# Performance work log

Measured on AMD Instinct MI355X. Metric: run time of the kernel, lower is better.

Reference implementation:

```python
import jax, jax.numpy as jnp
import numpy as np

SUB_NO, T_NO, T_DATA, E_NO, I_NO = 20, 201, 100000, 800, 200


def _build_c_den():
    # binary-tree dendrite topology: children of node p are 2p+1, 2p+2 (indices > parent,
    # so the reverse-order recursion in forward() is valid)
    C = np.zeros((SUB_NO, SUB_NO), np.float32)
    for p in range(SUB_NO):
        for c in (2 * p + 1, 2 * p + 2):
            if c < SUB_NO:
                C[p, c] = 1.0
    return jnp.asarray(C)


def setup_inputs() -> dict:
    key = jax.random.key(0)
    ks = jax.random.split(key, 8)
    S_e = jax.random.uniform(ks[0], (T_DATA, E_NO), dtype=jnp.float32)
    S_i = jax.random.uniform(ks[1], (T_DATA, I_NO), dtype=jnp.float32)
    # one-hot synapse -> subunit assignment matrices (fixed, greedy=False)
    ae = jax.random.randint(ks[2], (E_NO,), 0, SUB_NO)
    ai = jax.random.randint(ks[3], (I_NO,), 0, SUB_NO)
    C_syn_e = jax.nn.one_hot(ae, SUB_NO, dtype=jnp.float32).T  # (sub_no, E_no)
    C_syn_i = jax.nn.one_hot(ai, SUB_NO, dtype=jnp.float32).T  # (sub_no, I_no)
    W_syn = jax.random.uniform(ks[4], (SUB_NO, 2, 2), dtype=jnp.float32) * 0.05
    W_syn = W_syn.at[:, :, 1].multiply(-1.0)  # inhibitory weights negative
    Tau_syn = jnp.tile(jnp.array([1.1, 3.1], jnp.float32).reshape(1, 2, 1), (SUB_NO, 1, 2))
    Delta_syn = jax.random.uniform(ks[5], (SUB_NO, 2, 2), dtype=jnp.float32)
    W_sub = jax.random.uniform(ks[6], (SUB_NO,), dtype=jnp.float32)
    Theta = jnp.zeros((SUB_NO,), jnp.float32)
    V_o = jax.random.normal(ks[7], (1,), dtype=jnp.float32)
    return {"S_e": S_e, "S_i": S_i, "C_syn_e": C_syn_e, "C_syn_i": C_syn_i,
            "C_den": _build_c_den(), "W_syn": W_syn, "Tau_syn": Tau_syn,
            "Delta_syn": Delta_syn, "W_sub": W_sub, "Theta": Theta, "V_o": V_o}


def _alpha_kernels(W_syn, Tau_syn, Delta_syn):
    # sum of 2 alpha functions per subunit, separately for e (c=0) and i (c=1)
    t = jnp.arange(T_NO, dtype=jnp.float32)
    td = jnp.maximum(t[None, None, None, :] - Delta_syn[..., None], 0.0)  # (sub,2,2,T_no)
    tt = td / jnp.exp(Tau_syn)[..., None]
    part = tt * jnp.exp(-tt) * W_syn[..., None]
    kern = part.sum(axis=1)  # sum over the 2 alpha components -> (sub,2,T_no)
    return kern[:, 0, :], kern[:, 1, :]  # e_kern, i_kern each (sub, T_no)


def _causal_grouped_conv(syn, kern):
    # syn: (T, sub), kern: (sub, T_no). Matches torch: flip kernel, left-pad T_no-1 zeros,
    # grouped valid cross-correlation -> causal conv, output (T, sub).
    sub, T_no = kern.shape
    x = jnp.pad(syn.T, ((0, 0), (T_no - 1, 0)))[None]      # (1, sub, T+T_no-1)
    k = jnp.flip(kern, 1)[:, None, :]                       # (sub, 1, T_no)
    y = jax.lax.conv_general_dilated(x, k, (1,), 'VALID',
                                     dimension_numbers=('NCH', 'OIH', 'NCH'),
                                     feature_group_count=sub)
    return y[0].T


def reference(S_e, S_i, C_syn_e, C_syn_i, C_den, W_syn, Tau_syn, Delta_syn, W_sub, Theta, V_o):
    syn_e = S_e @ C_syn_e.T  # (T, sub) aggregated excitatory input
    syn_i = S_i @ C_syn_i.T
    e_kern, i_kern = _alpha_kernels(W_syn, Tau_syn, Delta_syn)
    syn_in = _causal_grouped_conv(syn_e, e_kern) + _causal_grouped_conv(syn_i, i_kern)
    # dendritic tree recursion, leaves (high idx) to root (idx 0).
    # leaf gather/sum expressed as a masked matvec with the binary C_den row
    # (exactly equal to the original gather since C_den is 0/1).
    W_exp = jnp.exp(W_sub)
    sub_no = C_den.shape[0]
    sub_out = jnp.zeros_like(syn_in)  # (T, sub)
    for s in range(sub_no - 1, -1, -1):
        leaf_sum = sub_out @ (C_den[s] * W_exp)  # (T,)
        sub_out = sub_out.at[:, s].set(jnp.tanh(syn_in[:, s] + leaf_sum + Theta[s]))
    final_voltage = sub_out[:, 0] * W_exp[0] + V_o  # (T,) via broadcast of V_o[1]
    out_filters = jnp.vstack((e_kern, i_kern))  # double flip in torch cancels
    return final_voltage, out_filters, C_syn_e, C_syn_i
```

## Files before the change

kernel.cpp:

```cpp
#include <hip/hip_runtime.h>
#include <hip/hip_bf16.h>
#include <stdint.h>

constexpr int T    = 100000;
constexpr int TNO  = 201;
constexpr int KP   = 204;
constexpr int NSUB = 20;
constexpr int ENO  = 800;
constexpr int INO  = 200;
constexpr int NCS  = 40;

constexpr int OUT_FILT = T;
constexpr int OUT_CSE  = OUT_FILT + NCS * TNO;

constexpr int WS_KFLIP = 0;
constexpr int WS_OFFE  = 32640;
constexpr int WS_OFFI  = 32768;
constexpr int WS_PERME = 32896;
constexpr int WS_PERMI = 36096;
constexpr int WS_SYN   = 36928;
constexpr size_t WS_NEEDED_SPLIT = (size_t)WS_SYN + (size_t)NCS * T * 4;

__device__ __forceinline__ float u16f(unsigned short u) {
  return __uint_as_float((unsigned int)u << 16);
}
__device__ __forceinline__ float ldany(const void* p, int i, int f32) {
  return f32 ? ((const float*)p)[i] : u16f(((const unsigned short*)p)[i]);
}
__device__ __forceinline__ void stany(void* p, int i, float v, int f32) {
  if (f32) ((float*)p)[i] = v;
  else     ((__hip_bfloat16*)p)[i] = __float2bfloat16(v);
}
__device__ __forceinline__ float safe_tanh(float x) {
  return 1.f - 2.f / (expf(2.f * x) + 1.f);
}

__device__ __forceinline__ int detect_f32(const void* Se) {
  const uint32_t w = ((const uint32_t*)Se)[threadIdx.x & 63];
  return (__ballot((w & 0x8000u) != 0u) != 0ull) ? 1 : 0;
}

__global__ __launch_bounds__(256) void kern_setup(
    const void* __restrict__ Se,
    const void* __restrict__ Wsyn,
    const void* __restrict__ Tau,
    const void* __restrict__ Delta,
    const void* __restrict__ Cse,
    const void* __restrict__ Csi,
    void* __restrict__ out,
    float* __restrict__ kflip,
    int* __restrict__ offE, int* __restrict__ offI,
    int* __restrict__ permE, int* __restrict__ permI)
{
  __shared__ int cnt[NSUB], offsh[NSUB + 1], pos[ENO], asg[ENO];

  const int f32 = detect_f32(Se);
  const int tid = threadIdx.x;
  const int cs  = blockIdx.x;
  const int s   = cs % NSUB;
  const int c   = cs / NSUB;

  if (tid <= 200) {
    const float tau = (float)tid;
    float v = 0.f;
#pragma unroll
    for (int j = 0; j < 2; ++j) {
      const float W  = ldany(Wsyn , (s * 2 + j) * 2 + c, f32);
      const float Tu = ldany(Tau  , (s * 2 + j) * 2 + c, f32);
      const float De = ldany(Delta, (s * 2 + j) * 2 + c, f32);
      const float td = fmaxf(tau - De, 0.f);
      const float tt = td / expf(Tu);
      v += tt * expf(-tt) * W;
    }
    stany(out, OUT_FILT + cs * TNO + tid, v, f32);
    kflip[cs * KP + (200 - tid)] = v;
  } else if (tid < KP) {
    kflip[cs * KP + tid] = 0.f;
  }

  for (int idx = blockIdx.x * 256 + tid; idx < NSUB * (ENO + INO); idx += 40 * 256) {
    const float v = (idx < NSUB * ENO) ? ldany(Cse, idx, f32)
                                       : ldany(Csi, idx - NSUB * ENO, f32);
    stany(out, OUT_CSE + idx, v, f32);
  }

  if (blockIdx.x == 0) {
    if (tid < NSUB) cnt[tid] = 0;
    __syncthreads();
    for (int e = tid; e < ENO; e += 256) {
      int a = 0;
      for (int ss = 0; ss < NSUB; ++ss)
        if (ldany(Cse, ss * ENO + e, f32) > 0.5f) a = ss;
      asg[e] = a;
      pos[e] = atomicAdd(&cnt[a], 1);
    }
    __syncthreads();
    if (tid == 0) {
      int acc = 0;
      for (int ss = 0; ss < NSUB; ++ss) { offsh[ss] = acc; acc += cnt[ss]; }
      offsh[NSUB] = acc;
    }
    __syncthreads();
    if (tid <= NSUB) offE[tid] = offsh[tid];
    for (int e = tid; e < ENO; e += 256) permE[offsh[asg[e]] + pos[e]] = e;
    __syncthreads();
    if (tid < NSUB) cnt[tid] = 0;
    __syncthreads();
    for (int e = tid; e < INO; e += 256) {
      int a = 0;
      for (int ss = 0; ss < NSUB; ++ss)
        if (ldany(Csi, ss * INO + e, f32) > 0.5f) a = ss;
      asg[e] = a;
      pos[e] = atomicAdd(&cnt[a], 1);
    }
    __syncthreads();
    if (tid == 0) {
      int acc = 0;
      for (int ss = 0; ss < NSUB; ++ss) { offsh[ss] = acc; acc += cnt[ss]; }
      offsh[NSUB] = acc;
    }
    __syncthreads();
    if (tid <= NSUB) offI[tid] = offsh[tid];
    for (int e = tid; e < INO; e += 256) permI[offsh[asg[e]] + pos[e]] = e;
  }
}

constexpr int AR   = 8;
constexpr int FSTR = 1004;
constexpr int BSTR = 504;

__global__ __launch_bounds__(256) void kern_agg(
    const void* __restrict__ Se,
    const void* __restrict__ Si,
    const int* __restrict__ offE, const int* __restrict__ offI,
    const int* __restrict__ permE, const int* __restrict__ permI,
    float* __restrict__ syn)
{
  __shared__ alignas(16) uint32_t lds[AR * FSTR];
  __shared__ int sOffE[NSUB + 1], sOffI[NSUB + 1];
  __shared__ int sPermE[ENO], sPermI[INO];

  const int f32 = detect_f32(Se);
  const int tid = threadIdx.x;
  const int t0  = blockIdx.x * AR;

  for (int i = tid; i < ENO; i += 256) sPermE[i] = permE[i];
  for (int i = tid; i < INO; i += 256) sPermI[i] = permI[i];
  if (tid <= NSUB) { sOffE[tid] = offE[tid]; sOffI[tid] = offI[tid]; }

  if (f32) {
    const float4* gE4 = (const float4*)Se + (size_t)t0 * 200;
    const float4* gI4 = (const float4*)Si + (size_t)t0 * 50;
#pragma unroll
    for (int u = 0; u < 7; ++u) {
      const int idx = tid + u * 256;
      float4 v; int w;
      if (idx < 1600) { v = gE4[idx]; const int r = idx / 200;
                        w = r * FSTR + (idx - r * 200) * 4; }
      else            { const int j = idx - 1600; v = gI4[j]; const int r = j / 50;
                        w = r * FSTR + 800 + (j - r * 50) * 4; }
      *(float4*)&lds[w] = v;
    }
    {
      const int idx = tid + 1792;
      if (idx < 2000) {
        const int j = idx - 1600;
        const int r = j / 50;
        *(float4*)&lds[r * FSTR + 800 + (j - r * 50) * 4] = gI4[j];
      }
    }
  } else {
    const uint32_t* gE = (const uint32_t*)Se + (size_t)t0 * 400;
    const uint32_t* gI = (const uint32_t*)Si + (size_t)t0 * 100;
    for (int idx = tid; idx < AR * 500; idx += 256) {
      const int r = idx / 500;
      const int w = idx - r * 500;
      lds[r * BSTR + w] = (w < 400) ? gE[r * 400 + w] : gI[r * 100 + (w - 400)];
    }
  }
  __syncthreads();

  for (int task = tid; task < NCS * AR; task += 256) {
    const int cs = task >> 3, r = task & 7;
    float v = 0.f;
    if (f32) {
      const float* row = (const float*)lds + r * FSTR;
      if (cs < NSUB) {
        const int b0 = sOffE[cs], b1 = sOffE[cs + 1];
#pragma unroll 4
        for (int k = b0; k < b1; ++k) v += row[sPermE[k]];
      } else {
        const int ss = cs - NSUB;
        const int b0 = sOffI[ss], b1 = sOffI[ss + 1];
#pragma unroll 4
        for (int k = b0; k < b1; ++k) v += row[800 + sPermI[k]];
      }
    } else {
      const unsigned short* row = (const unsigned short*)lds + r * (BSTR * 2);
      if (cs < NSUB) {
        const int b0 = sOffE[cs], b1 = sOffE[cs + 1];
        for (int k = b0; k < b1; ++k) v += u16f(row[sPermE[k]]);
      } else {
        const int ss = cs - NSUB;
        const int b0 = sOffI[ss], b1 = sOffI[ss + 1];
        for (int k = b0; k < b1; ++k) v += u16f(row[800 + sPermI[k]]);
      }
    }
    syn[(size_t)cs * T + t0 + r] = v;
  }
}

template<int TTC, int SBSC>
__device__ __forceinline__ void conv_tree_core(
    float* sybuf, const float* __restrict__ kflip,
    const float* __restrict__ wexpS, const float* __restrict__ thetaS,
    const void* __restrict__ Vo,
    void* __restrict__ out, int t0, int tid, int f32)
{
  constexpr int GRP   = TTC / 4;
  constexpr int NTASK = NCS * GRP;
  constexpr int NPASS = NTASK / 640;
  static_assert(NTASK % 640 == 0, "task count must tile 640 threads");

  float acc[NPASS][4];
#pragma unroll
  for (int pass = 0; pass < NPASS; ++pass) {
    const int task = tid + pass * 640;
    const int cs   = task / GRP;
    const int r0   = (task % GRP) << 2;
    const float*  xb = &sybuf[cs * SBSC + r0];
    const float4* kf = (const float4*)(kflip + cs * KP);
    float4 cur = *(const float4*)xb;
    float a0 = 0.f, a1 = 0.f, a2 = 0.f, a3 = 0.f;
    for (int jb = 0; jb < KP; jb += 4) {
      const float4 nxt = *(const float4*)(xb + jb + 4);
      const float4 k   = kf[jb >> 2];
      a0 = fmaf(k.x, cur.x, a0); a1 = fmaf(k.x, cur.y, a1);
      a2 = fmaf(k.x, cur.z, a2); a3 = fmaf(k.x, cur.w, a3);
      a0 = fmaf(k.y, cur.y, a0); a1 = fmaf(k.y, cur.z, a1);
      a2 = fmaf(k.y, cur.w, a2); a3 = fmaf(k.y, nxt.x, a3);
      a0 = fmaf(k.z, cur.z, a0); a1 = fmaf(k.z, cur.w, a1);
      a2 = fmaf(k.z, nxt.x, a2); a3 = fmaf(k.z, nxt.y, a3);
      a0 = fmaf(k.w, cur.w, a0); a1 = fmaf(k.w, nxt.x, a1);
      a2 = fmaf(k.w, nxt.y, a2); a3 = fmaf(k.w, nxt.z, a3);
      cur = nxt;
    }
    acc[pass][0] = a0; acc[pass][1] = a1; acc[pass][2] = a2; acc[pass][3] = a3;
  }
  __syncthreads();
#pragma unroll
  for (int pass = 0; pass < NPASS; ++pass) {
    const int task = tid + pass * 640;
    const int cs   = task / GRP;
    const int r0   = (task % GRP) << 2;
    sybuf[cs * SBSC + r0 + 0] = acc[pass][0];
    sybuf[cs * SBSC + r0 + 1] = acc[pass][1];
    sybuf[cs * SBSC + r0 + 2] = acc[pass][2];
    sybuf[cs * SBSC + r0 + 3] = acc[pass][3];
  }
  __syncthreads();

  if (tid < TTC) {
    const int t = t0 + tid;
    if (t < T) {
      float so[NSUB];
#pragma unroll
      for (int ss = NSUB - 1; ss >= 0; --ss) {
        float x = sybuf[ss * SBSC + tid] + sybuf[(NSUB + ss) * SBSC + tid]
                + thetaS[ss];
        if (2 * ss + 1 < NSUB) x += wexpS[2 * ss + 1] * so[2 * ss + 1];
        if (2 * ss + 2 < NSUB) x += wexpS[2 * ss + 2] * so[2 * ss + 2];
        so[ss] = safe_tanh(x);
      }
      stany(out, t, so[0] * wexpS[0] + ldany(Vo, 0, f32), f32);
    }
  }
}

constexpr int TT2 = 128;
constexpr int SB2 = 336;

__global__ __launch_bounds__(640) void kern_conv_tree(
    const void* __restrict__ Se,
    const float* __restrict__ kflip,
    const float* __restrict__ syn,
    const void* __restrict__ Wsub,
    const void* __restrict__ ThetaP,
    const void* __restrict__ Vo,
    void* __restrict__ out)
{
  __shared__ alignas(16) float sybuf[NCS * SB2];
  __shared__ float wexpS[NSUB], thetaS[NSUB];
  const int f32 = detect_f32(Se);
  const int tid = threadIdx.x;
  const int t0  = blockIdx.x * TT2;

  if (tid < NSUB) {
    wexpS[tid]  = expf(ldany(Wsub, tid, f32));
    thetaS[tid] = ldany(ThetaP, tid, f32);
  }
  for (int idx = tid; idx < NCS * (TT2 + KP); idx += 640) {
    const int cs = idx / (TT2 + KP);
    const int i  = idx - cs * (TT2 + KP);
    const int g  = t0 - 200 + i;
    float v = 0.f;
    if (g >= 0 && g < T) v = syn[(size_t)cs * T + g];
    sybuf[cs * SB2 + i] = v;
  }
  __syncthreads();
  conv_tree_core<TT2, SB2>(sybuf, kflip, wexpS, thetaS, Vo, out, t0, tid, f32);
}

constexpr int TT1 = 64;
constexpr int SB1 = 272;

__global__ __launch_bounds__(640) void kern_fused(
    const void* __restrict__ Se,
    const void* __restrict__ Si,
    const float* __restrict__ kflip,
    const int* __restrict__ offE, const int* __restrict__ offI,
    const int* __restrict__ permE, const int* __restrict__ permI,
    const void* __restrict__ Wsub,
    const void* __restrict__ ThetaP,
    const void* __restrict__ Vo,
    void* __restrict__ out)
{
  __shared__ alignas(16) float    sybuf[NCS * SB1];
  __shared__ alignas(16) uint32_t stage[4008];
  __shared__ float wexpS[NSUB], thetaS[NSUB];
  __shared__ int sOffE[NSUB + 1], sOffI[NSUB + 1];
  __shared__ int sPermE[ENO], sPermI[INO];

  const int f32 = detect_f32(Se);
  const int tid = threadIdx.x;
  const int t0  = blockIdx.x * TT1;

  for (int i = tid; i < ENO; i += 640) sPermE[i] = permE[i];
  for (int i = tid; i < INO; i += 640) sPermI[i] = permI[i];
  if (tid <= NSUB) { sOffE[tid] = offE[tid]; sOffI[tid] = offI[tid]; }
  if (tid < NSUB) {
    wexpS[tid]  = expf(ldany(Wsub, tid, f32));
    thetaS[tid] = ldany(ThetaP, tid, f32);
  }

  if (!f32) {
    const uint32_t* SeU = (const uint32_t*)Se;
    const uint32_t* SiU = (const uint32_t*)Si;
    for (int c = 0; c < 34; ++c) {
      const int g0 = t0 - 200 + c * 8;
      for (int idx = tid; idx < 8 * 500; idx += 640) {
        const int r = idx / 500;
        const int w = idx - r * 500;
        const int g = g0 + r;
        uint32_t v = 0u;
        if (g >= 0 && g < T)
          v = (w < 400) ? SeU[(size_t)g * 400 + w] : SiU[(size_t)g * 100 + (w - 400)];
        stage[r * 501 + w] = v;
      }
      __syncthreads();
      if (tid < 320) {
        const int isI = tid >= 160;
        const int t2  = isI ? tid - 160 : tid;
        const int ss  = t2 >> 3, r = t2 & 7;
        const int i   = c * 8 + r;
        const unsigned short* row = (const unsigned short*)(stage + r * 501);
        float v = 0.f;
        if (!isI) {
          for (int k = sOffE[ss]; k < sOffE[ss + 1]; ++k) v += u16f(row[sPermE[k]]);
          sybuf[ss * SB1 + i] = v;
        } else {
          row += 800;
          for (int k = sOffI[ss]; k < sOffI[ss + 1]; ++k) v += u16f(row[sPermI[k]]);
          sybuf[(NSUB + ss) * SB1 + i] = v;
        }
      }
      __syncthreads();
    }
  } else {
    const uint32_t* SeU = (const uint32_t*)Se;
    const uint32_t* SiU = (const uint32_t*)Si;
    for (int c = 0; c < 68; ++c) {
      const int g0 = t0 - 200 + c * 4;
      for (int idx = tid; idx < 4 * 1000; idx += 640) {
        const int r = idx / 1000;
        const int w = idx - r * 1000;
        const int g = g0 + r;
        uint32_t v = 0u;
        if (g >= 0 && g < T)
          v = (w < 800) ? SeU[(size_t)g * 800 + w] : SiU[(size_t)g * 200 + (w - 800)];
        stage[r * 1001 + w] = v;
      }
      __syncthreads();
      if (tid < 160) {
        const int isI = tid >= 80;
        const int t2  = isI ? tid - 80 : tid;
        const int ss  = t2 >> 2, r = t2 & 3;
        const int i   = c * 4 + r;
        const float* row = (const float*)(stage + r * 1001);
        float v = 0.f;
        if (!isI) {
          for (int k = sOffE[ss]; k < sOffE[ss + 1]; ++k) v += row[sPermE[k]];
          sybuf[ss * SB1 + i] = v;
        } else {
          row += 800;
          for (int k = sOffI[ss]; k < sOffI[ss + 1]; ++k) v += row[sPermI[k]];
          sybuf[(NSUB + ss) * SB1 + i] = v;
        }
      }
      __syncthreads();
    }
  }
  conv_tree_core<TT1, SB1>(sybuf, kflip, wexpS, thetaS, Vo, out, t0, tid, f32);
}

extern "C" void kernel_launch(void* const* d_in, const int* in_sizes, int n_in,
                              void* d_out, int out_size, void* d_ws, size_t ws_size,
                              hipStream_t stream)
{
  const void* Se    = d_in[0];
  const void* Si    = d_in[1];
  const void* Cse   = d_in[2];
  const void* Csi   = d_in[3];
  const void* Wsyn  = d_in[5];
  const void* Tau   = d_in[6];
  const void* Delta = d_in[7];
  const void* Wsub  = d_in[8];
  const void* Theta = d_in[9];
  const void* Vo    = d_in[10];

  char* ws = (char*)d_ws;
  float* kflip = (float*)(ws + WS_KFLIP);
  int*   offE  = (int*)(ws + WS_OFFE);
  int*   offI  = (int*)(ws + WS_OFFI);
  int*   permE = (int*)(ws + WS_PERME);
  int*   permI = (int*)(ws + WS_PERMI);
  float* syn   = (float*)(ws + WS_SYN);

  kern_setup<<<dim3(NCS), dim3(256), 0, stream>>>(
      Se, Wsyn, Tau, Delta, Cse, Csi, d_out, kflip, offE, offI, permE, permI);

  if (ws_size >= WS_NEEDED_SPLIT) {
    kern_agg<<<dim3(T / AR), dim3(256), 0, stream>>>(
        Se, Si, offE, offI, permE, permI, syn);
    kern_conv_tree<<<dim3((T + TT2 - 1) / TT2), dim3(640), 0, stream>>>(
        Se, kflip, syn, Wsub, Theta, Vo, d_out);
  } else {
    kern_fused<<<dim3((T + TT1 - 1) / TT1), dim3(640), 0, stream>>>(
        Se, Si, kflip, offE, offI, permE, permI, Wsub, Theta, Vo, d_out);
  }
}
```

Measured before the change: 629.5 us.

## Make aggregation kernel persistent with register prefetch and in-block permutation build

The aggregation kernel becomes a persistent grid of 1024 blocks that loop over time tiles. In the f32 path each block prefetches the next tile into registers while it reduces the current tile from LDS. Each block now builds the synapse permutation tables itself from the assignment matrices, which removes the dependency on the setup kernel's single-block permutation work; the setup kernel skips that work when the split path is taken. The trade-off is redundant per-block permutation construction (800x20 scans of Cse) plus higher register pressure from the 8 float4 prefetch registers.

New measurement: 693.2 us. 10.1% more time.

```diff
diff --git a/kernel.cpp b/kernel.cpp
--- a/kernel.cpp
+++ b/kernel.cpp
@@ -50,7 +50,8 @@
     void* __restrict__ out,
     float* __restrict__ kflip,
     int* __restrict__ offE, int* __restrict__ offI,
-    int* __restrict__ permE, int* __restrict__ permI)
+    int* __restrict__ permE, int* __restrict__ permI,
+    int buildPerm)
 {
   __shared__ int cnt[NSUB], offsh[NSUB + 1], pos[ENO], asg[ENO];
 
@@ -84,7 +85,7 @@
     stany(out, OUT_CSE + idx, v, f32);
   }
 
-  if (blockIdx.x == 0) {
+  if (blockIdx.x == 0 && buildPerm) {
     if (tid < NSUB) cnt[tid] = 0;
     __syncthreads();
     for (int e = tid; e < ENO; e += 256) {
@@ -125,88 +126,150 @@
   }
 }
 
-constexpr int AR   = 8;
-constexpr int FSTR = 1004;
-constexpr int BSTR = 504;
+constexpr int AR     = 8;
+constexpr int FSTR   = 1004;
+constexpr int BSTR   = 504;
+constexpr int NTILES = T / AR;
+constexpr int AGG_BLOCKS = 1024;
 
 __global__ __launch_bounds__(256) void kern_agg(
     const void* __restrict__ Se,
     const void* __restrict__ Si,
-    const int* __restrict__ offE, const int* __restrict__ offI,
-    const int* __restrict__ permE, const int* __restrict__ permI,
+    const void* __restrict__ Cse,
+    const void* __restrict__ Csi,
     float* __restrict__ syn)
 {
   __shared__ alignas(16) uint32_t lds[AR * FSTR];
   __shared__ int sOffE[NSUB + 1], sOffI[NSUB + 1];
   __shared__ int sPermE[ENO], sPermI[INO];
+  __shared__ int cnt[NSUB];
 
   const int f32 = detect_f32(Se);
   const int tid = threadIdx.x;
-  const int t0  = blockIdx.x * AR;
-
-  for (int i = tid; i < ENO; i += 256) sPermE[i] = permE[i];
-  for (int i = tid; i < INO; i += 256) sPermI[i] = permI[i];
-  if (tid <= NSUB) { sOffE[tid] = offE[tid]; sOffI[tid] = offI[tid]; }
+
+  int* asg = (int*)lds;
+  int* pos = (int*)lds + 1024;
+  if (tid < NSUB) cnt[tid] = 0;
+  __syncthreads();
+  for (int e = tid; e < ENO; e += 256) {
+    int a = 0;
+    for (int ss = 0; ss < NSUB; ++ss)
+      if (ldany(Cse, ss * ENO + e, f32) > 0.5f) a = ss;
+    asg[e] = a;
+    pos[e] = atomicAdd(&cnt[a], 1);
+  }
+  __syncthreads();
+  if (tid == 0) {
+    int acc = 0;
+    for (int ss = 0; ss < NSUB; ++ss) { sOffE[ss] = acc; acc += cnt[ss]; }
+    sOffE[NSUB] = acc;
+  }
+  __syncthreads();
+  for (int e = tid; e < ENO; e += 256) sPermE[sOffE[asg[e]] + pos[e]] = e;
+  __syncthreads();
+  if (tid < NSUB) cnt[tid] = 0;
+  __syncthreads();
+  for (int e = tid; e < INO; e += 256) {
+    int a = 0;
+    for (int ss = 0; ss < NSUB; ++ss)
+      if (ldany(Csi, ss * INO + e, f32) > 0.5f) a = ss;
+    asg[e] = a;
+    pos[e] = atomicAdd(&cnt[a], 1);
+  }
+  __syncthreads();
+  if (tid == 0) {
+    int acc = 0;
+    for (int ss = 0; ss < NSUB; ++ss) { sOffI[ss] = acc; acc += cnt[ss]; }
+    sOffI[NSUB] = acc;
+  }
+  __syncthreads();
+  for (int e = tid; e < INO; e += 256) sPermI[sOffI[asg[e]] + pos[e]] = e;
 
   if (f32) {
-    const float4* gE4 = (const float4*)Se + (size_t)t0 * 200;
-    const float4* gI4 = (const float4*)Si + (size_t)t0 * 50;
-#pragma unroll
-    for (int u = 0; u < 7; ++u) {
-      const int idx = tid + u * 256;
-      float4 v; int w;
-      if (idx < 1600) { v = gE4[idx]; const int r = idx / 200;
-                        w = r * FSTR + (idx - r * 200) * 4; }
-      else            { const int j = idx - 1600; v = gI4[j]; const int r = j / 50;
-                        w = r * FSTR + 800 + (j - r * 50) * 4; }
-      *(float4*)&lds[w] = v;
-    }
+    float4 v[8];
+    int tile = blockIdx.x;
     {
-      const int idx = tid + 1792;
-      if (idx < 2000) {
-        const int j = idx - 1600;
-        const int r = j / 50;
-        *(float4*)&lds[r * FSTR + 800 + (j - r * 50) * 4] = gI4[j];
-      }
+      const float4* gE4 = (const float4*)Se + (size_t)tile * (AR * 200);
+      const float4* gI4 = (const float4*)Si + (size_t)tile * (AR * 50);
+#pragma unroll
+      for (int u = 0; u < 8; ++u) {
+        const int idx = tid + u * 256;
+        if (idx < 1600)      v[u] = gE4[idx];
+        else if (idx < 2000) v[u] = gI4[idx - 1600];
+      }
+    }
+    while (tile < NTILES) {
+      const int t0 = tile * AR;
+      __syncthreads();
+#pragma unroll
+      for (int u = 0; u < 8; ++u) {
+        const int idx = tid + u * 256;
+        if (idx < 1600) {
+          const int r = idx / 200;
+          *(float4*)&lds[r * FSTR + (idx - r * 200) * 4] = v[u];
+        } else if (idx < 2000) {
+          const int j = idx - 1600;
+          const int r = j / 50;
+          *(float4*)&lds[r * FSTR + 800 + (j - r * 50) * 4] = v[u];
+        }
+      }
+      __syncthreads();
+      const int ntile = tile + AGG_BLOCKS;
+      if (ntile < NTILES) {
+        const float4* gE4 = (const float4*)Se + (size_t)ntile * (AR * 200);
+        const float4* gI4 = (const float4*)Si + (size_t)ntile * (AR * 50);
+#pragma unroll
+        for (int u = 0; u < 8; ++u) {
+          const int idx = tid + u * 256;
+          if (idx < 1600)      v[u] = gE4[idx];
+          else if (idx < 2000) v[u] = gI4[idx - 1600];
+        }
+      }
+      for (int task = tid; task < NCS * AR; task += 256) {
+        const int cs = task >> 3, r = task & 7;
+        const float* row = (const float*)lds + r * FSTR;
+        float vv = 0.f;
+        if (cs < NSUB) {
+          const int b0 = sOffE[cs], b1 = sOffE[cs + 1];
+#pragma unroll 4
+          for (int k = b0; k < b1; ++k) vv += row[sPermE[k]];
+        } else {
+          const int ss = cs - NSUB;
+          const int b0 = sOffI[ss], b1 = sOffI[ss + 1];
+#pragma unroll 4
+          for (int k = b0; k < b1; ++k) vv += row[800 + sPermI[k]];
+        }
+        syn[(size_t)cs * T + t0 + r] = vv;
+      }
+      tile = ntile;
     }
   } else {
-    const uint32_t* gE = (const uint32_t*)Se + (size_t)t0 * 400;
-    const uint32_t* gI = (const uint32_t*)Si + (size_t)t0 * 100;
-    for (int idx = tid; idx < AR * 500; idx += 256) {
-      const int r = idx / 500;
-      const int w = idx - r * 500;
-      lds[r * BSTR + w] = (w < 400) ? gE[r * 400 + w] : gI[r * 100 + (w - 400)];
-    }
-  }
-  __syncthreads();
-
-  for (int task = tid; task < NCS * AR; task += 256) {
-    const int cs = task >> 3, r = task & 7;
-    float v = 0.f;
-    if (f32) {
-      const float* row = (const float*)lds + r * FSTR;
-      if (cs < NSUB) {
-        const int b0 = sOffE[cs], b1 = sOffE[cs + 1];
-#pragma unroll 4
-        for (int k = b0; k < b1; ++k) v += row[sPermE[k]];
-      } else {
-        const int ss = cs - NSUB;
-        const int b0 = sOffI[ss], b1 = sOffI[ss + 1];
-#pragma unroll 4
-        for (int k = b0; k < b1; ++k) v += row[800 + sPermI[k]];
-      }
-    } else {
-      const unsigned short* row = (const unsigned short*)lds + r * (BSTR * 2);
-      if (cs < NSUB) {
-        const int b0 = sOffE[cs], b1 = sOffE[cs + 1];
-        for (int k = b0; k < b1; ++k) v += u16f(row[sPermE[k]]);
-      } else {
-        const int ss = cs - NSUB;
-        const int b0 = sOffI[ss], b1 = sOffI[ss + 1];
-        for (int k = b0; k < b1; ++k) v += u16f(row[800 + sPermI[k]]);
-      }
-    }
-    syn[(size_t)cs * T + t0 + r] = v;
+    for (int tile = blockIdx.x; tile < NTILES; tile += AGG_BLOCKS) {
+      const int t0 = tile * AR;
+      __syncthreads();
+      const uint32_t* gE = (const uint32_t*)Se + (size_t)t0 * 400;
+      const uint32_t* gI = (const uint32_t*)Si + (size_t)t0 * 100;
+      for (int idx = tid; idx < AR * 500; idx += 256) {
+        const int r = idx / 500;
+        const int w = idx - r * 500;
+        lds[r * BSTR + w] = (w < 400) ? gE[r * 400 + w] : gI[r * 100 + (w - 400)];
+      }
+      __syncthreads();
+      for (int task = tid; task < NCS * AR; task += 256) {
+        const int cs = task >> 3, r = task & 7;
+        const unsigned short* row = (const unsigned short*)lds + r * (BSTR * 2);
+        float vv = 0.f;
+        if (cs < NSUB) {
+          const int b0 = sOffE[cs], b1 = sOffE[cs + 1];
+          for (int k = b0; k < b1; ++k) vv += u16f(row[sPermE[k]]);
+        } else {
+          const int ss = cs - NSUB;
+          const int b0 = sOffI[ss], b1 = sOffI[ss + 1];
+          for (int k = b0; k < b1; ++k) vv += u16f(row[800 + sPermI[k]]);
+        }
+        syn[(size_t)cs * T + t0 + r] = vv;
+      }
+    }
   }
 }
 
@@ -436,12 +499,14 @@
   int*   permI = (int*)(ws + WS_PERMI);
   float* syn   = (float*)(ws + WS_SYN);
 
+  const int split = (ws_size >= WS_NEEDED_SPLIT) ? 1 : 0;
+
   kern_setup<<<dim3(NCS), dim3(256), 0, stream>>>(
-      Se, Wsyn, Tau, Delta, Cse, Csi, d_out, kflip, offE, offI, permE, permI);
-
-  if (ws_size >= WS_NEEDED_SPLIT) {
-    kern_agg<<<dim3(T / AR), dim3(256), 0, stream>>>(
-        Se, Si, offE, offI, permE, permI, syn);
+      Se, Wsyn, Tau, Delta, Cse, Csi, d_out, kflip, offE, offI, permE, permI,
+      split ? 0 : 1);
+
+  if (split) {
+    kern_agg<<<dim3(AGG_BLOCKS), dim3(256), 0, stream>>>(Se, Si, Cse, Csi, syn);
     kern_conv_tree<<<dim3((T + TT2 - 1) / TT2), dim3(640), 0, stream>>>(
         Se, kflip, syn, Wsub, Theta, Vo, d_out);
   } else {
```
